# Kernel tuning notes

Measured on AMD Instinct MI355X. Metric: run time of the kernel, lower is better.

## Reference

```python
import jax, jax.numpy as jnp
import numpy as np
from math import pi

TWO_PI = 2.0 * pi

def ringify(x):
    return (x + pi) % TWO_PI - pi

def complex_mean(x, axes):
    dir_x = ringify(jnp.cos(x)).sum(axis=axes)
    dir_y = jnp.sin(x).sum(axis=axes)
    return jnp.arctan2(dir_y, dir_x)

def extract_patches(x, k, s):
    # x: (B, C, H, W) -> (B, Ho, Wo, C, k, k)
    B, C, H, W = x.shape
    Ho = (H - k) // s + 1
    Wo = (W - k) // s + 1
    idx_h = jnp.arange(Ho)[:, None] * s + jnp.arange(k)[None, :]  # (Ho, k)
    idx_w = jnp.arange(Wo)[:, None] * s + jnp.arange(k)[None, :]  # (Wo, k)
    # advanced indexing on dims 2,3 with broadcast shape (Ho, Wo, k, k)
    p = x[:, :, idx_h[:, None, :, None], idx_w[None, :, None, :]]  # (B, C, Ho, Wo, k, k)
    return p.transpose(0, 2, 3, 1, 4, 5)

def ring_conv2d(x, weight, kernel_size, stride):
    # x: (B, C, H, W); weight: (O, C, k, k) -> out: (B, Ho, Wo, O)
    patches = extract_patches(x, kernel_size, stride)            # (B,Ho,Wo,C,k,k)
    w = weight.transpose(1, 2, 3, 0)                              # (C,k,k,O)
    diff = ringify(patches[..., None] - w)                        # (B,Ho,Wo,C,k,k,O)
    return complex_mean(diff, axes=(-4, -3, -2))                  # (B,Ho,Wo,O)

def setup_inputs() -> dict:
    key = jax.random.key(0)
    k1, k2, k3, k4 = jax.random.split(key, 4)
    return {
        "x": jax.random.normal(k1, (4096, 1, 28, 28), dtype=jnp.float32),
        "conv1_weight": jax.random.normal(k2, (4, 1, 2, 2), dtype=jnp.float32),
        "conv2_weight": jax.random.normal(k3, (8, 4, 4, 4), dtype=jnp.float32),
        "ff_weight": jax.random.normal(k4, (288, 10), dtype=jnp.float32),
    }

def reference(x, conv1_weight, conv2_weight, ff_weight):
    h = ringify(x).reshape(-1, 1, 28, 28)
    h = ring_conv2d(h, conv1_weight, kernel_size=2, stride=2)     # (B,14,14,4)
    h = h.transpose(0, 3, 1, 2)                                   # (B,4,14,14)
    h = ring_conv2d(h, conv2_weight, kernel_size=4, stride=2)     # (B,6,6,8)
    h = h.reshape(h.shape[0], -1)                                 # (B,288)
    h = complex_mean(ringify(h[:, :, None] - ff_weight), axes=(-2,))  # (B,10)
    return jnp.sin(h)
```

## Files before the change

### kernel.cpp

```cpp
#include <hip/hip_runtime.h>

#define WT_W1 0
#define WT_W2 16
#define WT_FF 528

typedef _Float16 h2 __attribute__((ext_vector_type(2)));

__device__ __forceinline__ float fdot2(unsigned a, unsigned b, float c) {
    return __builtin_amdgcn_fdot2(__builtin_bit_cast(h2, a),
                                  __builtin_bit_cast(h2, b), c, false);
}
__device__ __forceinline__ unsigned packh2(float x, float y) {
    h2 h; h.x = (_Float16)x; h.y = (_Float16)y;
    return __builtin_bit_cast(unsigned, h);
}

__global__ void ringnn_setup(const float* __restrict__ w1,
                             const float* __restrict__ w2,
                             const float* __restrict__ ffw,
                             uint2* __restrict__ wt) {
    int t = blockIdx.x * blockDim.x + threadIdx.x;
    if (t >= 3408) return;
    float a;
    if (t < 16)        a = w1[t];
    else if (t < 528)  a = w2[t - 16];
    else               a = ffw[t - 528];
    float s, c;
    __sincosf(a, &s, &c);
    uint2 v;
    v.x = packh2(c, s);
    v.y = packh2(-s, c);
    wt[t] = v;
}

__global__ __launch_bounds__(256) void ringnn_main(
    const float* __restrict__ x,
    const uint2* __restrict__ wt,
    float* __restrict__ out)
{
    __shared__ uint2 w1t[16];
    __shared__ uint4 w2t[264];
    __shared__ unsigned cs1[2][784];
    __shared__ unsigned cs2[2][288];

    const int t   = threadIdx.x;
    const int img = t >> 7;
    const int tid = t & 127;
    const int b   = blockIdx.x * 2 + img;
    const float* xb = x + b * 784;

    for (int k = t; k < 528; k += 256) {
        uint2 val = wt[k];
        if (k < 16) {
            w1t[k] = val;
        } else {
            int kk = k - 16;
            int o = kk >> 6, rest = kk & 63;
            ((uint2*)w2t)[o * 66 + rest] = val;
        }
    }
    __syncthreads();

    for (int pos = tid; pos < 196; pos += 128) {
        const int i = pos / 14;
        const int j = pos - i * 14;
        const float* px = xb + (2 * i) * 28 + 2 * j;
        float2 p0 = *(const float2*)(px);
        float2 p1 = *(const float2*)(px + 28);
        float s0, c0, s1, c1, s2, c2, s3, c3;
        __sincosf(p0.x, &s0, &c0);
        __sincosf(p0.y, &s1, &c1);
        __sincosf(p1.x, &s2, &c2);
        __sincosf(p1.y, &s3, &c3);
        unsigned v0 = packh2(c0, s0), v1 = packh2(c1, s1);
        unsigned v2 = packh2(c2, s2), v3 = packh2(c3, s3);
        #pragma unroll
        for (int o = 0; o < 4; ++o) {
            uint2 wa = w1t[o * 4 + 0], wb = w1t[o * 4 + 1];
            uint2 wc = w1t[o * 4 + 2], wd = w1t[o * 4 + 3];
            float X = 0.f, Y = 0.f;
            X = fdot2(v0, wa.x, X); Y = fdot2(v0, wa.y, Y);
            X = fdot2(v1, wb.x, X); Y = fdot2(v1, wb.y, Y);
            X = fdot2(v2, wc.x, X); Y = fdot2(v2, wc.y, Y);
            X = fdot2(v3, wd.x, X); Y = fdot2(v3, wd.y, Y);
            float rinv = rsqrtf(fmaxf(fmaf(X, X, Y * Y), 1e-30f));
            cs1[img][o * 196 + pos] = packh2(X * rinv, Y * rinv);
        }
    }
    __syncthreads();

    for (int idx = tid; idx < 288; idx += 128) {
        const int o   = idx & 7;
        const int pos = idx >> 3;
        const int i   = pos / 6;
        const int j   = pos - i * 6;
        const unsigned* cbase = &cs1[img][(2 * i) * 14 + 2 * j];
        const uint4*    wbase = &w2t[o * 33];
        float X0 = 0.f, Y0 = 0.f, X1 = 0.f, Y1 = 0.f;
        #pragma unroll
        for (int c = 0; c < 4; ++c) {
            float Xa = 0.f, Ya = 0.f;
            #pragma unroll
            for (int dy = 0; dy < 4; ++dy) {
                const unsigned* r = cbase + c * 196 + dy * 14;
                uint2 va = *(const uint2*)(r);
                uint2 vb = *(const uint2*)(r + 2);
                uint4 wA = wbase[c * 8 + dy * 2 + 0];
                uint4 wB = wbase[c * 8 + dy * 2 + 1];
                Xa = fdot2(va.x, wA.x, Xa); Ya = fdot2(va.x, wA.y, Ya);
                Xa = fdot2(va.y, wA.z, Xa); Ya = fdot2(va.y, wA.w, Ya);
                Xa = fdot2(vb.x, wB.x, Xa); Ya = fdot2(vb.x, wB.y, Ya);
                Xa = fdot2(vb.y, wB.z, Xa); Ya = fdot2(vb.y, wB.w, Ya);
            }
            if (c & 1) { X1 += Xa; Y1 += Ya; } else { X0 += Xa; Y0 += Ya; }
        }
        float X = X0 + X1, Y = Y0 + Y1;
        float rinv = rsqrtf(fmaxf(fmaf(X, X, Y * Y), 1e-30f));
        cs2[img][idx] = packh2(X * rinv, Y * rinv);
    }
    __syncthreads();

    float2* red = (float2*)cs1[img];
    {
        float X = 0.f, Y = 0.f;
        const int n = tid / 12;
        const int g = tid - n * 12;
        if (n < 10) {
            #pragma unroll 6
            for (int k = 0; k < 24; ++k) {
                const int f = g + 12 * k;
                unsigned v = cs2[img][f];
                uint2 wvv = wt[WT_FF + f * 10 + n];
                X = fdot2(v, wvv.x, X);
                Y = fdot2(v, wvv.y, Y);
            }
        }
        red[tid] = make_float2(X, Y);
    }
    __syncthreads();
    if (tid < 10) {
        float Xs = 0.f, Ys = 0.f;
        #pragma unroll
        for (int g2 = 0; g2 < 12; ++g2) {
            float2 p = red[tid * 12 + g2];
            Xs += p.x; Ys += p.y;
        }
        float rinv = rsqrtf(fmaxf(fmaf(Xs, Xs, Ys * Ys), 1e-30f));
        out[b * 10 + tid] = Ys * rinv;
    }
}

extern "C" void kernel_launch(void* const* d_in, const int* in_sizes, int n_in,
                              void* d_out, int out_size, void* d_ws, size_t ws_size,
                              hipStream_t stream) {
    const float* x   = (const float*)d_in[0];
    const float* w1  = (const float*)d_in[1];
    const float* w2  = (const float*)d_in[2];
    const float* ffw = (const float*)d_in[3];
    uint2* wt = (uint2*)d_ws;
    float* o  = (float*)d_out;

    ringnn_setup<<<14, 256, 0, stream>>>(w1, w2, ffw, wt);
    ringnn_main<<<2048, 256, 0, stream>>>(x, wt, o);
}
```

Measured before the change: 84.25 us.

## Read conv weights as wave-uniform scalar loads and reuse patch loads across outputs

Removes the shared-memory staging of conv1/conv2 weights and its barrier, and reads them directly from global memory. The output-channel index is made wave-uniform via readfirstlane, so the compiler can fetch the weights with scalar loads. Conv2 is restructured so each lane computes four output channels for one spatial position, loading each input patch from LDS once and reusing it across those channels. In exchange, only 36 of 64 lanes per wave are active in conv2, and register pressure rises from the four accumulator pairs.

```diff
diff --git a/kernel.cpp b/kernel.cpp
--- a/kernel.cpp
+++ b/kernel.cpp
@@ -38,28 +38,14 @@
     const uint2* __restrict__ wt,
     float* __restrict__ out)
 {
-    __shared__ uint2 w1t[16];
-    __shared__ uint4 w2t[264];
     __shared__ unsigned cs1[2][784];
     __shared__ unsigned cs2[2][288];
 
-    const int t   = threadIdx.x;
-    const int img = t >> 7;
-    const int tid = t & 127;
-    const int b   = blockIdx.x * 2 + img;
+    const int t    = threadIdx.x;
+    const int img  = t >> 7;
+    const int tid  = t & 127;
+    const int b    = blockIdx.x * 2 + img;
     const float* xb = x + b * 784;
-
-    for (int k = t; k < 528; k += 256) {
-        uint2 val = wt[k];
-        if (k < 16) {
-            w1t[k] = val;
-        } else {
-            int kk = k - 16;
-            int o = kk >> 6, rest = kk & 63;
-            ((uint2*)w2t)[o * 66 + rest] = val;
-        }
-    }
-    __syncthreads();
 
     for (int pos = tid; pos < 196; pos += 128) {
         const int i = pos / 14;
@@ -76,8 +62,8 @@
         unsigned v2 = packh2(c2, s2), v3 = packh2(c3, s3);
         #pragma unroll
         for (int o = 0; o < 4; ++o) {
-            uint2 wa = w1t[o * 4 + 0], wb = w1t[o * 4 + 1];
-            uint2 wc = w1t[o * 4 + 2], wd = w1t[o * 4 + 3];
+            uint2 wa = wt[WT_W1 + o * 4 + 0], wb = wt[WT_W1 + o * 4 + 1];
+            uint2 wc = wt[WT_W1 + o * 4 + 2], wd = wt[WT_W1 + o * 4 + 3];
             float X = 0.f, Y = 0.f;
             X = fdot2(v0, wa.x, X); Y = fdot2(v0, wa.y, Y);
             X = fdot2(v1, wb.x, X); Y = fdot2(v1, wb.y, Y);
@@ -89,34 +75,57 @@
     }
     __syncthreads();
 
-    for (int idx = tid; idx < 288; idx += 128) {
-        const int o   = idx & 7;
-        const int pos = idx >> 3;
-        const int i   = pos / 6;
-        const int j   = pos - i * 6;
-        const unsigned* cbase = &cs1[img][(2 * i) * 14 + 2 * j];
-        const uint4*    wbase = &w2t[o * 33];
-        float X0 = 0.f, Y0 = 0.f, X1 = 0.f, Y1 = 0.f;
-        #pragma unroll
-        for (int c = 0; c < 4; ++c) {
-            float Xa = 0.f, Ya = 0.f;
+    {
+        const int wave  = t >> 6;
+        const int lane  = t & 63;
+        const int img2  = wave >> 1;
+        const int ohalf = __builtin_amdgcn_readfirstlane(wave & 1);
+        if (lane < 36) {
+            const int i = lane / 6;
+            const int j = lane - i * 6;
+            const unsigned* cb = &cs1[img2][(2 * i) * 14 + 2 * j];
+            float X[4] = {0.f, 0.f, 0.f, 0.f};
+            float Y[4] = {0.f, 0.f, 0.f, 0.f};
             #pragma unroll
-            for (int dy = 0; dy < 4; ++dy) {
-                const unsigned* r = cbase + c * 196 + dy * 14;
-                uint2 va = *(const uint2*)(r);
-                uint2 vb = *(const uint2*)(r + 2);
-                uint4 wA = wbase[c * 8 + dy * 2 + 0];
-                uint4 wB = wbase[c * 8 + dy * 2 + 1];
-                Xa = fdot2(va.x, wA.x, Xa); Ya = fdot2(va.x, wA.y, Ya);
-                Xa = fdot2(va.y, wA.z, Xa); Ya = fdot2(va.y, wA.w, Ya);
-                Xa = fdot2(vb.x, wB.x, Xa); Ya = fdot2(vb.x, wB.y, Ya);
-                Xa = fdot2(vb.y, wB.z, Xa); Ya = fdot2(vb.y, wB.w, Ya);
+            for (int c = 0; c < 4; ++c) {
+                uint2 a[4][2];
+                #pragma unroll
+                for (int dy = 0; dy < 4; ++dy) {
+                    const unsigned* r = cb + c * 196 + dy * 14;
+                    a[dy][0] = *(const uint2*)(r);
+                    a[dy][1] = *(const uint2*)(r + 2);
+                }
+                #pragma unroll
+                for (int oo = 0; oo < 4; ++oo) {
+                    const uint2* wp = wt + WT_W2 + (ohalf * 4 + oo) * 64 + c * 16;
+                    #pragma unroll
+                    for (int dy = 0; dy < 4; ++dy) {
+                        uint2 w0 = wp[dy * 4 + 0], w1_ = wp[dy * 4 + 1];
+                        uint2 w2_ = wp[dy * 4 + 2], w3 = wp[dy * 4 + 3];
+                        unsigned va = a[dy][0].x, vb = a[dy][0].y;
+                        unsigned vc = a[dy][1].x, vd = a[dy][1].y;
+                        X[oo] = fdot2(va, w0.x, X[oo]); Y[oo] = fdot2(va, w0.y, Y[oo]);
+                        X[oo] = fdot2(vb, w1_.x, X[oo]); Y[oo] = fdot2(vb, w1_.y, Y[oo]);
+                        X[oo] = fdot2(vc, w2_.x, X[oo]); Y[oo] = fdot2(vc, w2_.y, Y[oo]);
+                        X[oo] = fdot2(vd, w3.x, X[oo]); Y[oo] = fdot2(vd, w3.y, Y[oo]);
+                    }
+                }
             }
-            if (c & 1) { X1 += Xa; Y1 += Ya; } else { X0 += Xa; Y0 += Ya; }
+            unsigned r0, r1, r2, r3;
+            {
+                float rv0 = rsqrtf(fmaxf(fmaf(X[0], X[0], Y[0] * Y[0]), 1e-30f));
+                float rv1 = rsqrtf(fmaxf(fmaf(X[1], X[1], Y[1] * Y[1]), 1e-30f));
+                float rv2 = rsqrtf(fmaxf(fmaf(X[2], X[2], Y[2] * Y[2]), 1e-30f));
+                float rv3 = rsqrtf(fmaxf(fmaf(X[3], X[3], Y[3] * Y[3]), 1e-30f));
+                r0 = packh2(X[0] * rv0, Y[0] * rv0);
+                r1 = packh2(X[1] * rv1, Y[1] * rv1);
+                r2 = packh2(X[2] * rv2, Y[2] * rv2);
+                r3 = packh2(X[3] * rv3, Y[3] * rv3);
+            }
+            uint2* dst = (uint2*)&cs2[img2][lane * 8 + ohalf * 4];
+            dst[0] = make_uint2(r0, r1);
+            dst[1] = make_uint2(r2, r3);
         }
-        float X = X0 + X1, Y = Y0 + Y1;
-        float rinv = rsqrtf(fmaxf(fmaf(X, X, Y * Y), 1e-30f));
-        cs2[img][idx] = packh2(X * rinv, Y * rinv);
     }
     __syncthreads();
 
```

Result: faster. 82.22 us (-2.4%).
